# Performance work log

Hardware: AMD Instinct MI355X
Metric: run time of the kernel (lower is better)

## Reference

```python
import jax, jax.numpy as jnp
import numpy as np

T, B, C = 2048, 8, 512
OUT = 512
NE = 16
TOPK = 2
LOSS_SCALE = 0.01
NEG_INF = 1.0e6  # module uses -1000000.0 for masked logits


def setup_inputs() -> dict:
    key = jax.random.key(0)
    k = jax.random.split(key, 4)
    a_assign = np.sqrt(6.0 / (C + NE)).astype(np.float32)  # xavier_uniform for Linear(C, NE)
    a_w1 = np.float32(np.sqrt(6.0) / (C + OUT))            # dynamic_init_method == 1
    return {
        "x": jax.random.normal(k[0], (T, B, C), dtype=jnp.float32),
        "assign_w": jax.random.uniform(k[1], (NE, C), minval=-a_assign, maxval=a_assign, dtype=jnp.float32),
        "assign_b": jnp.zeros((NE,), dtype=jnp.float32),
        "pw_w1": jax.random.uniform(k[2], (NE, OUT * C), minval=-a_w1, maxval=a_w1, dtype=jnp.float32),
        "bias_w": jnp.zeros((OUT, C), dtype=jnp.float32),  # pw_bias weight initialized to 0
        "bias_b": jnp.zeros((OUT,), dtype=jnp.float32),
    }


def reference(x, assign_w, assign_b, pw_w1, bias_w, bias_b):
    # key=None path of ConditionalDLFactorized18.forward, eval mode, tau=0 -> softmax gating.
    tokens = x.reshape(T * B, C)
    # Gating energies: Linear(key_dim, ne)
    energies = tokens @ assign_w.T + assign_b  # [TB, ne]
    # keeptopk_masked: set entries below k-th largest to -1e6
    topv, _ = jax.lax.top_k(energies, TOPK)
    energies = jnp.where(energies < topv[..., TOPK - 1:TOPK], -NEG_INF, energies)
    resp = jax.nn.softmax(energies, axis=-1)  # [TB, ne]
    # Importance/commitment loss (torch.std is unbiased -> ddof=1)
    importance = resp.sum(axis=0)  # [ne]
    loss = (LOSS_SCALE * jnp.std(importance, ddof=1) / jnp.mean(importance)).reshape(1)
    # Algebraically-equivalent reorder of (resp @ pw_w1).view(T,B,out,in) @ x:
    # apply each expert's matrix to the token first, then mix with resp.
    W = pw_w1.reshape(NE, OUT, C)
    expert_out = jnp.einsum("nc,eoc->neo", tokens, W)      # [TB, ne, out]
    y = jnp.einsum("ne,neo->no", resp, expert_out)          # [TB, out]
    y = y.reshape(T, B, OUT)
    # dynamic bias: pw_bias(x0) = x0 @ bias_w.T + bias_b
    y = y + x @ bias_w.T + bias_b
    return y, loss
```

## Files before the change

### kernel.cpp

```cpp
#include <hip/hip_runtime.h>
#include <hip/hip_bf16.h>

#define TB 16384
#define CDIM 512
#define OUTD 512
#define NE 16
#define NE_TOT 17
#define LOSS_SCALE 0.01f
#define BM 256
#define BN 128
#define BK 32
#define NSTEP 16
#define MAX_SCHED 80
#define MAXFLAG 8192
#define MARGIN 1e-3f
#define GATE_BLOCKS (TB / 64)
#define WCONV_BLOCKS ((NE_TOT * OUTD * CDIM / 4 + 255) / 256)

typedef __bf16 bf16_t;
typedef bf16_t bf16x8 __attribute__((ext_vector_type(8)));
typedef float f32x4 __attribute__((ext_vector_type(4)));
typedef unsigned short ushort4_t __attribute__((ext_vector_type(4)));
typedef unsigned short ushort8_t __attribute__((ext_vector_type(8)));

__device__ __forceinline__ unsigned short f2bf(float f) {
    unsigned int u = __float_as_uint(f);
    u += 0x7fffu + ((u >> 16) & 1u);
    return (unsigned short)(u >> 16);
}
__device__ __forceinline__ float bf2f(unsigned short h) {
    return __uint_as_float((unsigned int)h << 16);
}
__device__ __forceinline__ int sw4(int r) { return (r ^ (r >> 2)) & 3; }

__device__ __forceinline__ void async_copy16(void* lds, const void* g) {
    __builtin_amdgcn_global_load_lds(
        (const __attribute__((address_space(1))) unsigned int*)g,
        (__attribute__((address_space(3))) unsigned int*)lds, 16, 0, 0);
}

__global__ __launch_bounds__(256) void k_prep(
    const float* __restrict__ aw, unsigned short* __restrict__ awhl,
    int* cnt0, int* cnt1, float* importance, int* nflag, int* wflag)
{
    int t = threadIdx.x;
    if (t < NE) { cnt0[t] = 0; cnt1[t] = 0; importance[t] = 0.f; }
    if (t == 0) { *nflag = 0; *wflag = 0; }
    for (int i = t; i < NE * CDIM; i += 256) {
        float f = aw[i];
        unsigned short h = f2bf(f);
        float r = f - bf2f(h);
        awhl[i] = h;
        awhl[NE * CDIM + i] = f2bf(r);
    }
}

__global__ __launch_bounds__(256) void k_front(
    const float* __restrict__ x, const unsigned short* __restrict__ awhl,
    const float* __restrict__ ab, unsigned short* __restrict__ xbf,
    int* __restrict__ dec, float2* __restrict__ respd,
    int* __restrict__ flaglist, int* __restrict__ nflag, float* __restrict__ importance,
    int* __restrict__ cnt0, int* __restrict__ cnt1,
    const float* __restrict__ pw, const float* __restrict__ bw,
    unsigned short* __restrict__ wbf, int* __restrict__ wflag)
{
    int tid = threadIdx.x;
    if (blockIdx.x >= GATE_BLOCKS) {
        long i = (long)(blockIdx.x - GATE_BLOCKS) * 256 + tid;
        const long NPW = (long)NE * OUTD * CDIM / 4;
        const long NTOT = (long)NE_TOT * OUTD * CDIM / 4;
        if (i >= NTOT) return;
        const float* src = (i < NPW) ? (pw + i * 4) : (bw + (i - NPW) * 4);
        float4 v = *(const float4*)src;
        ushort4_t o;
        o[0] = f2bf(v.x); o[1] = f2bf(v.y); o[2] = f2bf(v.z); o[3] = f2bf(v.w);
        long row = i >> 7;
        int e0 = (int)(i & 127) * 4;
        int kt = e0 >> 5;
        int cc = (e0 >> 3) & 3;
        int half = e0 & 7;
        int ccs = cc ^ sw4((int)(row & 15));
        *(ushort4_t*)(wbf + row * CDIM + kt * 32 + ccs * 8 + half) = o;
        if (i >= NPW && (v.x != 0.f || v.y != 0.f || v.z != 0.f || v.w != 0.f))
            atomicOr(wflag, 1);
        return;
    }

    __shared__ float imp_s[NE];
    __shared__ int c0_s[NE], c1_s[NE];
    if (tid < NE) { imp_s[tid] = 0.f; c0_s[tid] = 0; c1_s[tid] = 0; }
    __syncthreads();

    int wv = tid >> 6, l = tid & 63;
    int n0 = blockIdx.x * 64 + wv * 16;
    int e = l & 15;
    int kg = l >> 4;

    const float* xrow = x + (size_t)(n0 + e) * CDIM + kg * 8;
    unsigned short* xbrow = xbf + (size_t)(n0 + e) * CDIM + kg * 8;
    const unsigned short* whiP = awhl + e * CDIM + kg * 8;
    const unsigned short* wloP = whiP + NE * CDIM;

    f32x4 acc = (f32x4){0.f, 0.f, 0.f, 0.f};
    #pragma unroll 4
    for (int ks = 0; ks < 16; ++ks) {
        float4 v0 = *(const float4*)(xrow + ks * 32);
        float4 v1 = *(const float4*)(xrow + ks * 32 + 4);
        ushort8_t hx, lx;
        #define CVT(idx, f) { unsigned short h_ = f2bf(f); hx[idx] = h_; \
                              float r_ = (f) - bf2f(h_); lx[idx] = f2bf(r_); }
        CVT(0, v0.x) CVT(1, v0.y) CVT(2, v0.z) CVT(3, v0.w)
        CVT(4, v1.x) CVT(5, v1.y) CVT(6, v1.z) CVT(7, v1.w)
        #undef CVT
        *(ushort8_t*)(xbrow + ks * 32) = hx;
        ushort8_t wh8 = *(const ushort8_t*)(whiP + ks * 32);
        ushort8_t wl8 = *(const ushort8_t*)(wloP + ks * 32);
        bf16x8 ah = *(bf16x8*)&hx, al = *(bf16x8*)&lx;
        bf16x8 bh = *(bf16x8*)&wh8, bl = *(bf16x8*)&wl8;
        acc = __builtin_amdgcn_mfma_f32_16x16x32_bf16(al, bh, acc, 0, 0, 0);
        acc = __builtin_amdgcn_mfma_f32_16x16x32_bf16(ah, bl, acc, 0, 0, 0);
        acc = __builtin_amdgcn_mfma_f32_16x16x32_bf16(ah, bh, acc, 0, 0, 0);
    }
    float bias = ab[e];
    f32x4 E;
    #pragma unroll
    for (int q = 0; q < 4; ++q) E[q] = acc[q] + bias;

    f32x4 m1 = E, m2, m3;
    #pragma unroll
    for (int q = 0; q < 4; ++q) { m2[q] = -3.4e38f; m3[q] = -3.4e38f; }
    #pragma unroll
    for (int off = 1; off <= 8; off <<= 1) {
        #pragma unroll
        for (int q = 0; q < 4; ++q) {
            float o1 = __shfl_xor(m1[q], off, 64);
            float o2 = __shfl_xor(m2[q], off, 64);
            float o3 = __shfl_xor(m3[q], off, 64);
            float M1 = fmaxf(m1[q], o1), x1 = fminf(m1[q], o1);
            float h2 = fmaxf(m2[q], o2), l2 = fminf(m2[q], o2);
            float M2 = fmaxf(x1, h2), x2 = fminf(x1, h2);
            float M3 = fmaxf(fmaxf(x2, l2), fmaxf(m3[q], o3));
            m1[q] = M1; m2[q] = M2; m3[q] = M3;
        }
    }
    f32x4 p, z;
    #pragma unroll
    for (int q = 0; q < 4; ++q) p[q] = (E[q] >= m2[q]) ? expf(E[q] - m1[q]) : 0.f;
    z = p;
    #pragma unroll
    for (int off = 1; off <= 8; off <<= 1)
        #pragma unroll
        for (int q = 0; q < 4; ++q) z[q] += __shfl_xor(z[q], off, 64);
    f32x4 resp;
    #pragma unroll
    for (int q = 0; q < 4; ++q) resp[q] = p[q] / z[q];

    int grp = l >> 4;
    int elo_q[4], ehi_q[4];
    float rlo_q[4], rhi_q[4];
    #pragma unroll
    for (int q = 0; q < 4; ++q) {
        unsigned long long mq = __ballot(p[q] > 0.f);
        unsigned int sub = (unsigned int)((mq >> (grp * 16)) & 0xffffULL);
        elo_q[q] = __builtin_ctz(sub);
        ehi_q[q] = 31 - __builtin_clz(sub);
        rlo_q[q] = __shfl(resp[q], grp * 16 + elo_q[q], 64);
        rhi_q[q] = __shfl(resp[q], grp * 16 + ehi_q[q], 64);
    }
    if ((l & 15) == 0) {
        #pragma unroll
        for (int q = 0; q < 4; ++q) {
            int n = n0 + grp * 4 + q;
            dec[n] = elo_q[q] | (ehi_q[q] << 8);
            respd[n] = make_float2(rlo_q[q], rhi_q[q]);
            atomicAdd(&c0_s[elo_q[q]], 1);
            atomicAdd(&c1_s[ehi_q[q]], 1);
            if (m2[q] - m3[q] < MARGIN) {
                int ix = atomicAdd(nflag, 1);
                if (ix < MAXFLAG) flaglist[ix] = n;
            }
        }
    }
    float s = resp[0] + resp[1] + resp[2] + resp[3];
    s += __shfl_xor(s, 16, 64);
    s += __shfl_xor(s, 32, 64);
    if (l < 16) atomicAdd(&imp_s[e], s);
    __syncthreads();
    if (tid < NE) {
        unsafeAtomicAdd(&importance[tid], imp_s[tid]);
        if (c0_s[tid]) atomicAdd(&cnt0[tid], c0_s[tid]);
        if (c1_s[tid]) atomicAdd(&cnt1[tid], c1_s[tid]);
    }
}

__global__ __launch_bounds__(256) void k_repair(
    const float* __restrict__ x, const float* __restrict__ aw, const float* __restrict__ ab,
    const int* __restrict__ flaglist, const int* __restrict__ nflag,
    int* __restrict__ dec, float2* __restrict__ respd, float* __restrict__ importance,
    int* __restrict__ cnt0, int* __restrict__ cnt1)
{
    __shared__ double part[16][17];
    __shared__ double Ed[16];
    int tid = threadIdx.x;
    int e = tid >> 4, p = tid & 15;
    int nf = *nflag; if (nf > MAXFLAG) nf = MAXFLAG;
    for (int fi = blockIdx.x; fi < nf; fi += gridDim.x) {
        int n = flaglist[fi];
        const float* xp_ = x + (size_t)n * CDIM + p * 32;
        const float* wp = aw + e * CDIM + p * 32;
        double acc = 0.0;
        for (int j = 0; j < 32; ++j) acc = fma((double)xp_[j], (double)wp[j], acc);
        part[e][p] = acc;
        __syncthreads();
        if (tid < 16) {
            double s = (double)ab[tid];
            for (int q = 0; q < 16; ++q) s += part[tid][q];
            Ed[tid] = s;
        }
        __syncthreads();
        if (tid == 0) {
            double m1 = -1e300, m2 = -1e300, m3 = -1e300;
            for (int q = 0; q < 16; ++q) {
                double v = Ed[q];
                if (v > m1) { m3 = m2; m2 = m1; m1 = v; }
                else if (v > m2) { m3 = m2; m2 = v; }
                else if (v > m3) { m3 = v; }
            }
            int elo = -1, ehi = -1;
            for (int q = 0; q < 16; ++q)
                if (Ed[q] >= m2) { if (elo < 0) elo = q; else ehi = q; }
            double plo = exp(Ed[elo] - m1), phi = exp(Ed[ehi] - m1);
            double zz = plo + phi;
            float rlo = (float)(plo / zz), rhi = (float)(phi / zz);
            int od = dec[n]; float2 orr = respd[n];
            int oelo = od & 0xff, oehi = (od >> 8) & 0xff;
            unsafeAtomicAdd(&importance[oelo], -orr.x);
            unsafeAtomicAdd(&importance[oehi], -orr.y);
            unsafeAtomicAdd(&importance[elo], rlo);
            unsafeAtomicAdd(&importance[ehi], rhi);
            if (oelo != elo) { atomicSub(&cnt0[oelo], 1); atomicAdd(&cnt0[elo], 1); }
            if (oehi != ehi) { atomicSub(&cnt1[oehi], 1); atomicAdd(&cnt1[ehi], 1); }
            dec[n] = elo | (ehi << 8);
            respd[n] = make_float2(rlo, rhi);
        }
        __syncthreads();
    }
}

__global__ void k_finish(const float* __restrict__ importance, float* __restrict__ out_loss,
                         const int* __restrict__ cnt0, const int* __restrict__ cnt1,
                         int* __restrict__ fill0, int* __restrict__ fill1,
                         int* __restrict__ end0a, int* __restrict__ end1a,
                         int* __restrict__ sched0, int* __restrict__ sched1,
                         int* __restrict__ sn0, int* __restrict__ sn1) {
    int l = threadIdx.x;
    if (l < 64) {
        float v = (l < NE) ? importance[l] : 0.f;
        float s = v;
        #pragma unroll
        for (int off = 8; off >= 1; off >>= 1) s += __shfl_xor(s, off, 64);
        float mean = s / 16.f;
        float d = (l < NE) ? (v - mean) : 0.f;
        float ss = d * d;
        #pragma unroll
        for (int off = 8; off >= 1; off >>= 1) ss += __shfl_xor(ss, off, 64);
        if (l == 0) {
            float stdv = sqrtf(ss / 15.f);
            out_loss[0] = LOSS_SCALE * stdv / mean;
        }
    } else if (l == 64) {
        int p = 0, base = 0;
        for (int e = 0; e < NE; ++e) {
            fill0[e] = base;
            end0a[e] = base + cnt0[e];
            int nb = (cnt0[e] + BM - 1) / BM;
            for (int i = 0; i < nb; ++i) sched0[p++] = (e << 20) | (base + i * BM);
            base += cnt0[e];
        }
        *sn0 = p;
    } else if (l == 65) {
        int p = 0, base = 0;
        for (int e = 0; e < NE; ++e) {
            fill1[e] = base;
            end1a[e] = base + cnt1[e];
            int nb = (cnt1[e] + BM - 1) / BM;
            for (int i = 0; i < nb; ++i) sched1[p++] = (e << 20) | (base + i * BM);
            base += cnt1[e];
        }
        *sn1 = p;
    }
}

__global__ __launch_bounds__(256) void k_scatter(
    const int* __restrict__ dec, int* __restrict__ fill0, int* __restrict__ fill1,
    int* __restrict__ idx0c, int* __restrict__ idx1c)
{
    __shared__ int l0[NE], l1[NE], b0[NE], b1[NE];
    int tid = threadIdx.x;
    if (tid < NE) { l0[tid] = 0; l1[tid] = 0; }
    __syncthreads();
    int n = blockIdx.x * 256 + tid;
    int d = dec[n];
    int elo = d & 0xff, ehi = (d >> 8) & 0xff;
    int p0 = atomicAdd(&l0[elo], 1);
    int p1 = atomicAdd(&l1[ehi], 1);
    __syncthreads();
    if (tid < NE) {
        b0[tid] = atomicAdd(&fill0[tid], l0[tid]);
        b1[tid] = atomicAdd(&fill1[tid], l1[tid]);
    }
    __syncthreads();
    idx0c[b0[elo] + p0] = n;
    idx1c[b1[ehi] + p1] = n;
}

template<int MODE>
__global__ __launch_bounds__(512) void k_gemm(
    const unsigned short* __restrict__ xbf, const unsigned short* __restrict__ wbf,
    const int* __restrict__ idxc, const float2* __restrict__ respd,
    const int* __restrict__ sched, const int* __restrict__ sn,
    const int* __restrict__ enda, const int* __restrict__ wflag,
    const float* __restrict__ bias_b, float* __restrict__ y)
{
    int e, m0, end;
    if (MODE == 2) {
        if (*wflag == 0) return;
        e = NE; m0 = blockIdx.x * BM; end = TB;
    } else {
        if ((int)blockIdx.x >= *sn) return;
        int s = sched[blockIdx.x];
        e = s >> 20; m0 = s & 0xFFFFF; end = enda[e];
    }
    int n0 = blockIdx.y * BN;
    int tid = threadIdx.x;
    int wave = tid >> 6, lane = tid & 63;
    int wm = wave >> 1, wn = wave & 1;
    int fr = lane & 15, fq = lane >> 4;

    __shared__ unsigned short As[2][BM * BK];
    __shared__ unsigned short Bs[2][BN * BK];

    f32x4 acc[4][4];
    #pragma unroll
    for (int m = 0; m < 4; ++m)
        #pragma unroll
        for (int nn = 0; nn < 4; ++nn) acc[m][nn] = (f32x4){0.f, 0.f, 0.f, 0.f};

    int rl = lane >> 2, cc = lane & 3;
    const unsigned short* aS[2];
    #pragma unroll
    for (int c = 0; c < 2; ++c) {
        int rloc = wave * 32 + c * 16 + rl;
        int tokr;
        if (MODE == 2) tokr = m0 + rloc;
        else { int rr = m0 + rloc; if (rr >= end) rr = end - 1; tokr = idxc[rr]; }
        aS[c] = xbf + (size_t)tokr * CDIM + (cc ^ sw4(rloc)) * 8;
    }
    const unsigned short* bS =
        wbf + ((size_t)e * OUTD + n0 + wave * 16 + rl) * CDIM + cc * 8;

    auto stage = [&](int buf, int t) {
        async_copy16(&As[buf][(wave * 32) * BK], aS[0] + t * BK);
        async_copy16(&As[buf][(wave * 32 + 16) * BK], aS[1] + t * BK);
        async_copy16(&Bs[buf][(wave * 16) * BK], bS + t * BK);
    };
    auto compute = [&](int cb) {
        bf16x8 af[4], bv[4];
        #pragma unroll
        for (int m = 0; m < 4; ++m) {
            int row = wm * 64 + m * 16 + fr;
            af[m] = *(const bf16x8*)(&As[cb][row * BK + ((fq ^ sw4(fr)) * 8)]);
        }
        #pragma unroll
        for (int nn = 0; nn < 4; ++nn) {
            int row = wn * 64 + nn * 16 + fr;
            bv[nn] = *(const bf16x8*)(&Bs[cb][row * BK + ((fq ^ sw4(fr)) * 8)]);
        }
        #pragma unroll
        for (int m = 0; m < 4; ++m)
            #pragma unroll
            for (int nn = 0; nn < 4; ++nn)
                acc[m][nn] = __builtin_amdgcn_mfma_f32_16x16x32_bf16(af[m], bv[nn], acc[m][nn], 0, 0, 0);
    };

    stage(0, 0); stage(1, 1);
    #pragma unroll
    for (int t = 0; t < NSTEP; ++t) {
        if (t < NSTEP - 1) asm volatile("s_waitcnt vmcnt(3)" ::: "memory");
        else               asm volatile("s_waitcnt vmcnt(0)" ::: "memory");
        __builtin_amdgcn_sched_barrier(0);
        __builtin_amdgcn_s_barrier();
        asm volatile("" ::: "memory");
        compute(t & 1);
        __builtin_amdgcn_s_barrier();
        asm volatile("" ::: "memory");
        if (t + 2 < NSTEP) stage(t & 1, t + 2);
    }

    float bb[4];
    if (MODE == 0) {
        #pragma unroll
        for (int nn = 0; nn < 4; ++nn) bb[nn] = bias_b[n0 + wn * 64 + nn * 16 + fr];
    }
    #pragma unroll
    for (int m = 0; m < 4; ++m)
        #pragma unroll
        for (int q = 0; q < 4; ++q) {
            int r = m0 + wm * 64 + m * 16 + fq * 4 + q;
            if (r < end) {
                int tok = (MODE == 2) ? r : idxc[r];
                float w = 1.f;
                if (MODE != 2) {
                    float2 rp = respd[tok];
                    w = (MODE == 0) ? rp.x : rp.y;
                }
                float* yrow = y + (size_t)tok * OUTD + n0 + wn * 64 + fr;
                #pragma unroll
                for (int nn = 0; nn < 4; ++nn) {
                    if (MODE == 0)      yrow[nn * 16] = fmaf(w, acc[m][nn][q], bb[nn]);
                    else if (MODE == 1) yrow[nn * 16] += w * acc[m][nn][q];
                    else                yrow[nn * 16] += acc[m][nn][q];
                }
            }
        }
}

extern "C" void kernel_launch(void* const* d_in, const int* in_sizes, int n_in,
                              void* d_out, int out_size, void* d_ws, size_t ws_size,
                              hipStream_t stream) {
    const float* x        = (const float*)d_in[0];
    const float* assign_w = (const float*)d_in[1];
    const float* assign_b = (const float*)d_in[2];
    const float* pw_w1    = (const float*)d_in[3];
    const float* bias_w   = (const float*)d_in[4];
    const float* bias_b   = (const float*)d_in[5];
    float* y    = (float*)d_out;
    float* loss = y + (size_t)TB * OUTD;

    char* ws = (char*)d_ws;
    unsigned short* wbf  = (unsigned short*)(ws);
    unsigned short* xbf  = (unsigned short*)(ws + 8912896);
    int*    idx0c     = (int*)   (ws + 25690112);
    int*    idx1c     = (int*)   (ws + 25755648);
    int*    dec       = (int*)   (ws + 25821184);
    float2* respd     = (float2*)(ws + 25886720);
    int*    flaglist  = (int*)   (ws + 26017792);
    unsigned short* awhl = (unsigned short*)(ws + 26050560);
    char*   misc      = ws + 26083328;
    int*    cnt0      = (int*)   (misc + 0);
    int*    cnt1      = (int*)   (misc + 64);
    int*    fill0     = (int*)   (misc + 128);
    int*    fill1     = (int*)   (misc + 192);
    int*    end0a     = (int*)   (misc + 256);
    int*    end1a     = (int*)   (misc + 320);
    float*  importance= (float*) (misc + 384);
    int*    nflag     = (int*)   (misc + 448);
    int*    wflag     = (int*)   (misc + 452);
    int*    sn0       = (int*)   (misc + 456);
    int*    sn1       = (int*)   (misc + 460);
    int*    sched0    = (int*)   (misc + 512);
    int*    sched1    = (int*)   (misc + 832);

    k_prep<<<1, 256, 0, stream>>>(assign_w, awhl, cnt0, cnt1, importance, nflag, wflag);
    k_front<<<GATE_BLOCKS + WCONV_BLOCKS, 256, 0, stream>>>(
        x, awhl, assign_b, xbf, dec, respd, flaglist, nflag, importance, cnt0, cnt1,
        pw_w1, bias_w, wbf, wflag);
    k_repair<<<32, 256, 0, stream>>>(x, assign_w, assign_b, flaglist, nflag,
                                     dec, respd, importance, cnt0, cnt1);
    k_finish<<<1, 128, 0, stream>>>(importance, loss, cnt0, cnt1, fill0, fill1,
                                    end0a, end1a, sched0, sched1, sn0, sn1);
    k_scatter<<<TB / 256, 256, 0, stream>>>(dec, fill0, fill1, idx0c, idx1c);
    k_gemm<0><<<dim3(MAX_SCHED, OUTD / BN), 512, 0, stream>>>(
        xbf, wbf, idx0c, respd, sched0, sn0, end0a, wflag, bias_b, y);
    k_gemm<1><<<dim3(MAX_SCHED, OUTD / BN), 512, 0, stream>>>(
        xbf, wbf, idx1c, respd, sched1, sn1, end1a, wflag, bias_b, y);
    k_gemm<2><<<dim3(TB / BM, OUTD / BN), 512, 0, stream>>>(
        xbf, wbf, idx1c, respd, sched1, sn1, end1a, wflag, bias_b, y);
}
```

Before: 106.6 us.

## Load GEMM operands directly from global into registers instead of via LDS

Drops the LDS-staged double-buffered async copy pipeline and its barriers in the expert GEMM. Each lane now loads its MFMA fragments straight from global memory into a two-deep register buffer. The weight conversion writes a plain row-major layout with no swizzle. This removes barrier and LDS traffic, but operands shared by the two waves of a block are no longer loaded once, so global and L2 load traffic roughly doubles and the accesses are less coalesced.

```diff
diff --git a/kernel.cpp b/kernel.cpp
--- a/kernel.cpp
+++ b/kernel.cpp
@@ -9,7 +9,6 @@
 #define LOSS_SCALE 0.01f
 #define BM 256
 #define BN 128
-#define BK 32
 #define NSTEP 16
 #define MAX_SCHED 80
 #define MAXFLAG 8192
@@ -30,13 +29,6 @@
 }
 __device__ __forceinline__ float bf2f(unsigned short h) {
     return __uint_as_float((unsigned int)h << 16);
-}
-__device__ __forceinline__ int sw4(int r) { return (r ^ (r >> 2)) & 3; }
-
-__device__ __forceinline__ void async_copy16(void* lds, const void* g) {
-    __builtin_amdgcn_global_load_lds(
-        (const __attribute__((address_space(1))) unsigned int*)g,
-        (__attribute__((address_space(3))) unsigned int*)lds, 16, 0, 0);
 }
 
 __global__ __launch_bounds__(256) void k_prep(
@@ -74,13 +66,7 @@
         float4 v = *(const float4*)src;
         ushort4_t o;
         o[0] = f2bf(v.x); o[1] = f2bf(v.y); o[2] = f2bf(v.z); o[3] = f2bf(v.w);
-        long row = i >> 7;
-        int e0 = (int)(i & 127) * 4;
-        int kt = e0 >> 5;
-        int cc = (e0 >> 3) & 3;
-        int half = e0 & 7;
-        int ccs = cc ^ sw4((int)(row & 15));
-        *(ushort4_t*)(wbf + row * CDIM + kt * 32 + ccs * 8 + half) = o;
+        *(ushort4_t*)(wbf + i * 4) = o;
         if (i >= NPW && (v.x != 0.f || v.y != 0.f || v.z != 0.f || v.w != 0.f))
             atomicOr(wflag, 1);
         return;
@@ -337,8 +323,18 @@
     int wm = wave >> 1, wn = wave & 1;
     int fr = lane & 15, fq = lane >> 4;
 
-    __shared__ unsigned short As[2][BM * BK];
-    __shared__ unsigned short Bs[2][BN * BK];
+    const unsigned short* aptr[4];
+    const unsigned short* bptr[4];
+    #pragma unroll
+    for (int i = 0; i < 4; ++i) {
+        int r = m0 + wm * 64 + i * 16 + fr;
+        int tok;
+        if (MODE == 2) tok = r;
+        else { int rr = r; if (rr >= end) rr = end - 1; tok = idxc[rr]; }
+        aptr[i] = xbf + (size_t)tok * CDIM + fq * 8;
+        int c = n0 + wn * 64 + i * 16 + fr;
+        bptr[i] = wbf + ((size_t)e * OUTD + c) * CDIM + fq * 8;
+    }
 
     f32x4 acc[4][4];
     #pragma unroll
@@ -346,55 +342,30 @@
         #pragma unroll
         for (int nn = 0; nn < 4; ++nn) acc[m][nn] = (f32x4){0.f, 0.f, 0.f, 0.f};
 
-    int rl = lane >> 2, cc = lane & 3;
-    const unsigned short* aS[2];
-    #pragma unroll
-    for (int c = 0; c < 2; ++c) {
-        int rloc = wave * 32 + c * 16 + rl;
-        int tokr;
-        if (MODE == 2) tokr = m0 + rloc;
-        else { int rr = m0 + rloc; if (rr >= end) rr = end - 1; tokr = idxc[rr]; }
-        aS[c] = xbf + (size_t)tokr * CDIM + (cc ^ sw4(rloc)) * 8;
-    }
-    const unsigned short* bS =
-        wbf + ((size_t)e * OUTD + n0 + wave * 16 + rl) * CDIM + cc * 8;
-
-    auto stage = [&](int buf, int t) {
-        async_copy16(&As[buf][(wave * 32) * BK], aS[0] + t * BK);
-        async_copy16(&As[buf][(wave * 32 + 16) * BK], aS[1] + t * BK);
-        async_copy16(&Bs[buf][(wave * 16) * BK], bS + t * BK);
-    };
-    auto compute = [&](int cb) {
-        bf16x8 af[4], bv[4];
-        #pragma unroll
-        for (int m = 0; m < 4; ++m) {
-            int row = wm * 64 + m * 16 + fr;
-            af[m] = *(const bf16x8*)(&As[cb][row * BK + ((fq ^ sw4(fr)) * 8)]);
-        }
-        #pragma unroll
-        for (int nn = 0; nn < 4; ++nn) {
-            int row = wn * 64 + nn * 16 + fr;
-            bv[nn] = *(const bf16x8*)(&Bs[cb][row * BK + ((fq ^ sw4(fr)) * 8)]);
-        }
+    bf16x8 av[2][4], bv[2][4];
+    #pragma unroll
+    for (int i = 0; i < 4; ++i) {
+        av[0][i] = *(const bf16x8*)(aptr[i]);
+        bv[0][i] = *(const bf16x8*)(bptr[i]);
+        av[1][i] = *(const bf16x8*)(aptr[i] + 32);
+        bv[1][i] = *(const bf16x8*)(bptr[i] + 32);
+    }
+
+    #pragma unroll
+    for (int t = 0; t < NSTEP; ++t) {
         #pragma unroll
         for (int m = 0; m < 4; ++m)
             #pragma unroll
             for (int nn = 0; nn < 4; ++nn)
-                acc[m][nn] = __builtin_amdgcn_mfma_f32_16x16x32_bf16(af[m], bv[nn], acc[m][nn], 0, 0, 0);
-    };
-
-    stage(0, 0); stage(1, 1);
-    #pragma unroll
-    for (int t = 0; t < NSTEP; ++t) {
-        if (t < NSTEP - 1) asm volatile("s_waitcnt vmcnt(3)" ::: "memory");
-        else               asm volatile("s_waitcnt vmcnt(0)" ::: "memory");
-        __builtin_amdgcn_sched_barrier(0);
-        __builtin_amdgcn_s_barrier();
-        asm volatile("" ::: "memory");
-        compute(t & 1);
-        __builtin_amdgcn_s_barrier();
-        asm volatile("" ::: "memory");
-        if (t + 2 < NSTEP) stage(t & 1, t + 2);
+                acc[m][nn] = __builtin_amdgcn_mfma_f32_16x16x32_bf16(
+                    av[t & 1][m], bv[t & 1][nn], acc[m][nn], 0, 0, 0);
+        if (t + 2 < NSTEP) {
+            #pragma unroll
+            for (int i = 0; i < 4; ++i) {
+                av[t & 1][i] = *(const bf16x8*)(aptr[i] + (t + 2) * 32);
+                bv[t & 1][i] = *(const bf16x8*)(bptr[i] + (t + 2) * 32);
+            }
+        }
     }
 
     float bb[4];
```

Result: slower. 209.0 us (+96.0%).
